# Performance work log

Hardware: AMD Instinct MI355X
Metric: run time of the kernel (lower is better)

The kernel has to match this reference:

```python
import jax, jax.numpy as jnp
import numpy as np

WIN = 4
HEAD_DIM = 32
N_HEADS = 6
TYPE = 'SW'
SHIFT = WIN // 2  # window_size // 2


def _relation():
    # [P, P, 3] relative coordinate indices into the (2w-1)^3 bias table
    cord = np.array([[i, j, k] for i in range(WIN) for j in range(WIN) for k in range(WIN)])
    return cord[:, None, :] - cord[None, :, :] + WIN - 1


def _shift_mask(nw):
    # boolean mask [nw^3, P, P]; True -> -inf (cross-boundary pairs in shifted windows)
    p, s = WIN, WIN - SHIFT
    m = np.zeros((nw, nw, nw, p, p, p, p, p, p), dtype=bool)
    m[-1, :, :, :s, :, :, s:, :, :] = True
    m[-1, :, :, s:, :, :, :s, :, :] = True
    m[:, -1, :, :, :s, :, :, s:, :] = True
    m[:, -1, :, :, s:, :, :, :s, :] = True
    m[:, :, -1, :, :, :s, :, :, s:] = True
    m[:, :, -1, :, :, s:, :, :, :s] = True
    return m.reshape(nw ** 3, p ** 3, p ** 3)


def setup_inputs() -> dict:
    key = jax.random.key(0)
    ks = jax.random.split(key, 6)
    dim = N_HEADS * HEAD_DIM  # 192
    B, S = 2, 32
    x = jax.random.normal(ks[0], (B, S, S, S, dim), jnp.float32)
    W_qkv = jax.random.normal(ks[1], (dim, 3 * dim), jnp.float32) * 0.02
    b_qkv = jnp.zeros((3 * dim,), jnp.float32)
    rel_params = jax.random.normal(ks[2], (N_HEADS, 2 * WIN - 1, 2 * WIN - 1, 2 * WIN - 1), jnp.float32) * 0.02
    W_out = jax.random.normal(ks[3], (dim, dim), jnp.float32) * 0.02
    b_out = jnp.zeros((dim,), jnp.float32)
    return {"x": x, "W_qkv": W_qkv, "b_qkv": b_qkv, "rel_params": rel_params, "W_out": W_out, "b_out": b_out}


def reference(x, W_qkv, b_qkv, rel_params, W_out, b_out):
    B, H, Wd, D, C = x.shape
    p = WIN
    nw = H // p
    scale = HEAD_DIM ** -0.5
    if TYPE != 'W':
        x = jnp.roll(x, (-SHIFT, -SHIFT, -SHIFT), axis=(1, 2, 3))
    # window partition: [B, NW, P, C], NW = nw^3, P = p^3
    xw = x.reshape(B, nw, p, nw, p, nw, p, C).transpose(0, 1, 3, 5, 2, 4, 6, 7).reshape(B, nw ** 3, p ** 3, C)
    qkv = xw @ W_qkv + b_qkv  # [B, NW, P, 3C]
    qkv = qkv.reshape(B, nw ** 3, p ** 3, 3 * N_HEADS, HEAD_DIM).transpose(3, 0, 1, 2, 4)  # [3h, B, NW, P, d]
    q, k, v = qkv[:N_HEADS], qkv[N_HEADS:2 * N_HEADS], qkv[2 * N_HEADS:]
    sim = jnp.einsum('hbwpc,hbwqc->hbwpq', q, k) * scale
    rel = _relation()
    bias = rel_params[:, rel[:, :, 0], rel[:, :, 1], rel[:, :, 2]]  # [h, P, P]
    sim = sim + bias[:, None, None, :, :]
    if TYPE != 'W':
        mask = jnp.asarray(_shift_mask(nw))[None, None]  # [1,1,NW,P,P]
        sim = jnp.where(mask, -jnp.inf, sim)
    probs = jax.nn.softmax(sim, axis=-1)
    out = jnp.einsum('hbwpq,hbwqc->hbwpc', probs, v)
    out = out.transpose(1, 2, 3, 0, 4).reshape(B, nw ** 3, p ** 3, C)  # h b w p c -> b w p (h c)
    out = out @ W_out + b_out
    out = out.reshape(B, nw, nw, nw, p, p, p, C).transpose(0, 1, 4, 2, 5, 3, 6, 7).reshape(B, H, Wd, D, C)
    if TYPE != 'W':
        out = jnp.roll(out, (SHIFT, SHIFT, SHIFT), axis=(1, 2, 3))
    return out
```

## Files before the change

### kernel.cpp

```cpp
#include <hip/hip_runtime.h>

typedef short bf16x8 __attribute__((ext_vector_type(8)));
typedef float f32x4 __attribute__((ext_vector_type(4)));

#define MFMA16(a, b, c) __builtin_amdgcn_mfma_f32_16x16x32_bf16(a, b, c, 0, 0, 0)

__device__ __forceinline__ unsigned short f2bf(float f) {
    unsigned int u = __float_as_uint(f);
    u += 0x7FFFu + ((u >> 16) & 1u);
    return (unsigned short)(u >> 16);
}
__device__ __forceinline__ unsigned int f2bf2(float a, float b) {
    unsigned int ua = __float_as_uint(a);
    ua += 0x7FFFu + ((ua >> 16) & 1u);
    unsigned int ub = __float_as_uint(b);
    ub += 0x7FFFu + ((ub >> 16) & 1u);
    return (ua >> 16) | (ub & 0xFFFF0000u);
}
#define DPPADD(v, CTRL)                                                        \
    {                                                                          \
        int _t = __builtin_amdgcn_mov_dpp(__float_as_int(v), CTRL, 0xf, 0xf, true); \
        v += __int_as_float(_t);                                               \
    }

#define WQT_OFF 0
#define WOT_OFF 221184
#define BQ_OFF  294912

__global__ void prep_kernel(const float* __restrict__ Wqkv,
                            const float* __restrict__ bqkv,
                            const float* __restrict__ Wout,
                            unsigned short* __restrict__ WqT,
                            unsigned short* __restrict__ WoT,
                            float* __restrict__ bq) {
    __shared__ float tile[32][33];
    const float SCALE = 0.17677669529663687f * 1.4426950408889634f;
    int bid = blockIdx.x;
    int tx = threadIdx.x & 31, ty = threadIdx.x >> 5;
    if (bid < 108) {
        int tn = bid % 18, tc = bid / 18;
#pragma unroll
        for (int i = 0; i < 4; ++i)
            tile[ty + i * 8][tx] = Wqkv[(tc * 32 + ty + i * 8) * 576 + tn * 32 + tx];
        __syncthreads();
        bool isQ = (tn < 6);
#pragma unroll
        for (int i = 0; i < 4; ++i) {
            float v = tile[tx][ty + i * 8];
            if (isQ) v *= SCALE;
            WqT[(tn * 32 + ty + i * 8) * 192 + tc * 32 + tx] = f2bf(v);
        }
    } else if (bid < 144) {
        int bb = bid - 108;
        int tn = bb % 6, tc = bb / 6;
#pragma unroll
        for (int i = 0; i < 4; ++i)
            tile[ty + i * 8][tx] = Wout[(tc * 32 + ty + i * 8) * 192 + tn * 32 + tx];
        __syncthreads();
#pragma unroll
        for (int i = 0; i < 4; ++i)
            WoT[(tn * 32 + ty + i * 8) * 192 + tc * 32 + tx] = f2bf(tile[tx][ty + i * 8]);
    } else {
        for (int i = threadIdx.x; i < 576; i += 256) {
            float v = bqkv[i];
            if (i < 192) v *= SCALE;
            bq[i] = v;
        }
    }
}

#define OFF_X   0
#define OFF_P   0
#define OFF_QK  13312
#define OFF_VT  38400
#define OFF_O   52224
#define OFF_RELF 65536
#define SMEM_US 69652

__global__ __launch_bounds__(512) void wmsa_kernel(
    const float* __restrict__ x, const float* __restrict__ rel,
    const float* __restrict__ bout,
    const unsigned short* __restrict__ WqT,
    const unsigned short* __restrict__ WoT,
    const float* __restrict__ bq, float* __restrict__ out) {
    __shared__ __align__(16) unsigned short smem[SMEM_US];
    float* sRel = (float*)&smem[OFF_RELF];

    const int tid = threadIdx.x;
    const int bw = blockIdx.x;
    const int b  = bw >> 9;
    const int w  = bw & 511;
    const int wz = w >> 6, wy = (w >> 3) & 7, wx = w & 7;

    const int lane = tid & 63;
    const int wv   = tid >> 6;
    const int g    = lane >> 4;
    const int l15  = lane & 15;

    for (int i = tid; i < 2058; i += 512) sRel[i] = rel[i] * 1.4426950408889634f;
    {
        int t = tid >> 3, q8 = tid & 7;
        int tz = t >> 4, ty = (t >> 2) & 3, tx = t & 3;
        int gz = (wz * 4 + tz + 2) & 31;
        int gy = (wy * 4 + ty + 2) & 31;
        int gx = (wx * 4 + tx + 2) & 31;
        const float* xp = x + ((((b * 32 + gz) * 32 + gy) * 32 + gx)) * 192;
#pragma unroll
        for (int k = 0; k < 6; ++k) {
            int c = (q8 << 2) + (k << 5);
            float4 v = *(const float4*)(xp + c);
            uint2 pk;
            pk.x = f2bf2(v.x, v.y);
            pk.y = f2bf2(v.z, v.w);
            *(uint2*)&smem[OFF_X + t * 208 + c] = pk;
        }
    }

    int nb = wv;
    float bias = bq[nb * 16 + l15];
    bf16x8 bfr[6];
    {
        const unsigned short* wp = WqT + (nb * 16 + l15) * 192 + g * 8;
#pragma unroll
        for (int kk = 0; kk < 6; ++kk) bfr[kk] = *(const bf16x8*)(wp + kk * 32);
    }
    __syncthreads();

    {
        bf16x8 afr[4][6];
#pragma unroll
        for (int m = 0; m < 4; ++m)
#pragma unroll
            for (int kk = 0; kk < 6; ++kk)
                afr[m][kk] = *(const bf16x8*)&smem[OFF_X + (m * 16 + l15) * 208 + kk * 32 + g * 8];

        while (true) {
            int nbN = nb + 8;
            bool more = (nbN < 36);
            bf16x8 bfrN[6];
            float biasN = 0.f;
            if (more) {
                biasN = bq[nbN * 16 + l15];
                const unsigned short* wp = WqT + (nbN * 16 + l15) * 192 + g * 8;
#pragma unroll
                for (int kk = 0; kk < 6; ++kk) bfrN[kk] = *(const bf16x8*)(wp + kk * 32);
            }
            int colg = nb * 16 + l15;
            bool isV = (nb >= 24);
#pragma unroll
            for (int m = 0; m < 4; ++m) {
                f32x4 acc = {bias, bias, bias, bias};
#pragma unroll
                for (int kk = 0; kk < 6; ++kk) acc = MFMA16(afr[m][kk], bfr[kk], acc);
                int row0 = m * 16 + g * 4;
                unsigned int u01 = f2bf2(acc[0], acc[1]);
                unsigned int u23 = f2bf2(acc[2], acc[3]);
                if (!isV) {
                    unsigned short* qk = &smem[OFF_QK + row0 * 392 + colg];
                    qk[0]    = (unsigned short)u01;
                    qk[392]  = (unsigned short)(u01 >> 16);
                    qk[784]  = (unsigned short)u23;
                    qk[1176] = (unsigned short)(u23 >> 16);
                } else {
                    uint2 pk; pk.x = u01; pk.y = u23;
                    *(uint2*)&smem[OFF_VT + (colg - 384) * 72 + row0] = pk;
                }
            }
            if (!more) break;
            nb = nbN;
            bias = biasN;
#pragma unroll
            for (int kk = 0; kk < 6; ++kk) bfr[kk] = bfrN[kk];
        }
    }
    __syncthreads();

    const bool sz = (wz == 7), sy = (wy == 7), sx = (wx == 7);
    {
        const int qy = (l15 >> 2) & 3, qx = l15 & 3;
        unsigned short* pb = &smem[OFF_P + wv * 1152];
        for (int it = wv * 3; it < wv * 3 + 3; ++it) {
            int h = it >> 2, mb = it & 3;
            bf16x8 qf = *(const bf16x8*)&smem[OFF_QK + (mb * 16 + l15) * 392 + h * 32 + g * 8];
            f32x4 s[4];
#pragma unroll
            for (int f = 0; f < 4; ++f) {
                bf16x8 kf = *(const bf16x8*)&smem[OFF_QK + (f * 16 + l15) * 392 + 192 + h * 32 + g * 8];
                f32x4 z = {0.f, 0.f, 0.f, 0.f};
                s[f] = MFMA16(qf, kf, z);
            }
#pragma unroll
            for (int f = 0; f < 4; ++f) {
                bool mz = sz && ((mb < 2) != (f < 2));
                bool my = sy && ((g < 2) != (qy < 2));
                int base = h * 343 + (mb - f + 3) * 49 + (g - qy + 3) * 7 + (3 - qx);
#pragma unroll
                for (int r = 0; r < 4; ++r) {
                    float v = s[f][r] + sRel[base + r];
                    bool mx = sx && ((r < 2) != (qx < 2));
                    v = (mz | my | mx) ? -1e30f : v;
                    s[f][r] = exp2f(v);
                }
            }
            float inv[4];
#pragma unroll
            for (int r = 0; r < 4; ++r) {
                float sm = (s[0][r] + s[1][r]) + (s[2][r] + s[3][r]);
                DPPADD(sm, 0xB1);
                DPPADD(sm, 0x4E);
                DPPADD(sm, 0x124);
                DPPADD(sm, 0x128);
                inv[r] = __builtin_amdgcn_rcpf(sm);
            }
#pragma unroll
            for (int f = 0; f < 4; ++f) {
                unsigned int u01 = f2bf2(s[f][0], s[f][1]);
                unsigned int u23 = f2bf2(s[f][2], s[f][3]);
                unsigned short* pw = &pb[(g * 4) * 72 + f * 16 + l15];
                pw[0]   = (unsigned short)u01;
                pw[72]  = (unsigned short)(u01 >> 16);
                pw[144] = (unsigned short)u23;
                pw[216] = (unsigned short)(u23 >> 16);
            }
            f32x4 o0 = {0.f, 0.f, 0.f, 0.f}, o1 = {0.f, 0.f, 0.f, 0.f};
#pragma unroll
            for (int kt = 0; kt < 2; ++kt) {
                bf16x8 pf = *(const bf16x8*)&pb[l15 * 72 + kt * 32 + g * 8];
                bf16x8 v0 = *(const bf16x8*)&smem[OFF_VT + (h * 32 + l15) * 72 + kt * 32 + g * 8];
                bf16x8 v1 = *(const bf16x8*)&smem[OFF_VT + (h * 32 + 16 + l15) * 72 + kt * 32 + g * 8];
                o0 = MFMA16(pf, v0, o0);
                o1 = MFMA16(pf, v1, o1);
            }
#pragma unroll
            for (int r = 0; r < 4; ++r) { o0[r] *= inv[r]; o1[r] *= inv[r]; }
            unsigned int a0 = f2bf2(o0[0], o0[1]), a1 = f2bf2(o0[2], o0[3]);
            unsigned int c0 = f2bf2(o1[0], o1[1]), c1 = f2bf2(o1[2], o1[3]);
            unsigned short* ow = &smem[OFF_O + (mb * 16 + g * 4) * 208 + h * 32 + l15];
            ow[0]        = (unsigned short)a0;
            ow[208]      = (unsigned short)(a0 >> 16);
            ow[416]      = (unsigned short)a1;
            ow[624]      = (unsigned short)(a1 >> 16);
            ow[16]       = (unsigned short)c0;
            ow[16 + 208] = (unsigned short)(c0 >> 16);
            ow[16 + 416] = (unsigned short)c1;
            ow[16 + 624] = (unsigned short)(c1 >> 16);
        }
    }

    const int mw = wv >> 2, nq = wv & 3;
    int col0 = nq * 16 + l15;
    float bo0 = bout[col0];
    bf16x8 bfr0[6];
    {
        const unsigned short* wp = WoT + col0 * 192 + g * 8;
#pragma unroll
        for (int kk = 0; kk < 6; ++kk) bfr0[kk] = *(const bf16x8*)(wp + kk * 32);
    }
    __syncthreads();

    {
        bf16x8 ofr[2][6];
#pragma unroll
        for (int mi = 0; mi < 2; ++mi)
#pragma unroll
            for (int kk = 0; kk < 6; ++kk)
                ofr[mi][kk] = *(const bf16x8*)&smem[OFF_O + ((mw * 2 + mi) * 16 + l15) * 208 + kk * 32 + g * 8];
#pragma unroll
        for (int nbi = 0; nbi < 3; ++nbi) {
            int col = (nq + nbi * 4) * 16 + l15;
            float bo;
            bf16x8 bfr[6];
            if (nbi == 0) {
                bo = bo0;
#pragma unroll
                for (int kk = 0; kk < 6; ++kk) bfr[kk] = bfr0[kk];
            } else {
                bo = bout[col];
                const unsigned short* wp = WoT + col * 192 + g * 8;
#pragma unroll
                for (int kk = 0; kk < 6; ++kk) bfr[kk] = *(const bf16x8*)(wp + kk * 32);
            }
#pragma unroll
            for (int mi = 0; mi < 2; ++mi) {
                f32x4 acc = {bo, bo, bo, bo};
#pragma unroll
                for (int kk = 0; kk < 6; ++kk) acc = MFMA16(ofr[mi][kk], bfr[kk], acc);
                int m = mw * 2 + mi;
                int gz = (wz * 4 + m + 2) & 31;
                int gy = (wy * 4 + g + 2) & 31;
#pragma unroll
                for (int r = 0; r < 4; ++r) {
                    int gx = (wx * 4 + r + 2) & 31;
                    out[(((b * 32 + gz) * 32 + gy) * 32 + gx) * 192 + col] = acc[r];
                }
            }
        }
    }
}

extern "C" void kernel_launch(void* const* d_in, const int* in_sizes, int n_in,
                              void* d_out, int out_size, void* d_ws, size_t ws_size,
                              hipStream_t stream) {
    const float* x    = (const float*)d_in[0];
    const float* Wqkv = (const float*)d_in[1];
    const float* bqkv = (const float*)d_in[2];
    const float* rel  = (const float*)d_in[3];
    const float* Wout = (const float*)d_in[4];
    const float* bout = (const float*)d_in[5];

    unsigned short* WqT = (unsigned short*)((char*)d_ws + WQT_OFF);
    unsigned short* WoT = (unsigned short*)((char*)d_ws + WOT_OFF);
    float*          bq  = (float*)((char*)d_ws + BQ_OFF);
    float*          out = (float*)d_out;

    prep_kernel<<<145, 256, 0, stream>>>(Wqkv, bqkv, Wout, WqT, WoT, bq);
    wmsa_kernel<<<1024, 512, 0, stream>>>(x, rel, bout, WqT, WoT, bq, out);
}
```

Baseline: 166.7 us.

## Precompute per-lane bias table, swap MFMA operands, shrink LDS for two blocks per CU

Adds a prep stage that expands the relative-position bias into a per-lane table in global memory, so each block no longer loads the rel table into LDS and the inner loop reads contiguous float4s. The QKV and output GEMMs swap MFMA operand order so accumulators map to contiguous columns, which gives vectorized LDS stores and float4 global output stores instead of scattered scalar stores. Softmax normalization moves before the PV product. X is stored in a fragment-friendly layout, and LDS use drops to allow two 512-thread blocks per CU via launch bounds. The cost is extra global bias-table traffic, per-block reads of that table, and tighter register limits.

```diff
diff --git a/kernel.cpp b/kernel.cpp
--- a/kernel.cpp
+++ b/kernel.cpp
@@ -26,14 +26,18 @@
 #define WQT_OFF 0
 #define WOT_OFF 221184
 #define BQ_OFF  294912
+#define TBL_OFF 297216
 
 __global__ void prep_kernel(const float* __restrict__ Wqkv,
                             const float* __restrict__ bqkv,
                             const float* __restrict__ Wout,
+                            const float* __restrict__ rel,
                             unsigned short* __restrict__ WqT,
                             unsigned short* __restrict__ WoT,
-                            float* __restrict__ bq) {
+                            float* __restrict__ bq,
+                            float* __restrict__ tblB) {
     __shared__ float tile[32][33];
+    const float LOG2E = 1.4426950408889634f;
     const float SCALE = 0.17677669529663687f * 1.4426950408889634f;
     int bid = blockIdx.x;
     int tx = threadIdx.x & 31, ty = threadIdx.x >> 5;
@@ -60,31 +64,36 @@
 #pragma unroll
         for (int i = 0; i < 4; ++i)
             WoT[(tn * 32 + ty + i * 8) * 192 + tc * 32 + tx] = f2bf(tile[tx][ty + i * 8]);
-    } else {
+    } else if (bid == 144) {
         for (int i = threadIdx.x; i < 576; i += 256) {
             float v = bqkv[i];
             if (i < 192) v *= SCALE;
             bq[i] = v;
         }
+    } else {
+        int e = (bid - 145) * 256 + threadIdx.x;
+        int r = e & 3, f = (e >> 2) & 3;
+        int lane = (e >> 4) & 63, mb = (e >> 10) & 3, h = e >> 12;
+        int g = lane >> 4, l15 = lane & 15;
+        int qy = l15 >> 2, qx = l15 & 3;
+        int dz = mb - f + 3, dy = g - qy + 3, dx = r - qx + 3;
+        tblB[e] = rel[((h * 7 + dz) * 7 + dy) * 7 + dx] * LOG2E;
     }
 }
 
 #define OFF_X   0
-#define OFF_P   0
-#define OFF_QK  13312
-#define OFF_VT  38400
-#define OFF_O   52224
-#define OFF_RELF 65536
-#define SMEM_US 69652
-
-__global__ __launch_bounds__(512) void wmsa_kernel(
-    const float* __restrict__ x, const float* __restrict__ rel,
+#define OFF_QK  12288
+#define OFF_VT  37376
+#define OFF_O   51200
+#define SMEM_US 64000
+
+__global__ __launch_bounds__(512, 2) void wmsa_kernel(
+    const float* __restrict__ x, const float* __restrict__ tblB,
     const float* __restrict__ bout,
     const unsigned short* __restrict__ WqT,
     const unsigned short* __restrict__ WoT,
     const float* __restrict__ bq, float* __restrict__ out) {
     __shared__ __align__(16) unsigned short smem[SMEM_US];
-    float* sRel = (float*)&smem[OFF_RELF];
 
     const int tid = threadIdx.x;
     const int bw = blockIdx.x;
@@ -97,7 +106,6 @@
     const int g    = lane >> 4;
     const int l15  = lane & 15;
 
-    for (int i = tid; i < 2058; i += 512) sRel[i] = rel[i] * 1.4426950408889634f;
     {
         int t = tid >> 3, q8 = tid & 7;
         int tz = t >> 4, ty = (t >> 2) & 3, tx = t & 3;
@@ -105,80 +113,86 @@
         int gy = (wy * 4 + ty + 2) & 31;
         int gx = (wx * 4 + tx + 2) & 31;
         const float* xp = x + ((((b * 32 + gz) * 32 + gy) * 32 + gx)) * 192;
+        int g0 = q8 >> 1, j0 = (q8 & 1) * 4, lt = t & 15;
 #pragma unroll
         for (int k = 0; k < 6; ++k) {
-            int c = (q8 << 2) + (k << 5);
-            float4 v = *(const float4*)(xp + c);
+            float4 v = *(const float4*)(xp + q8 * 4 + k * 32);
             uint2 pk;
             pk.x = f2bf2(v.x, v.y);
             pk.y = f2bf2(v.z, v.w);
-            *(uint2*)&smem[OFF_X + t * 208 + c] = pk;
+            *(uint2*)&smem[OFF_X + ((((k * 4 + g0) * 4 + tz) * 16 + lt) * 8) + j0] = pk;
         }
     }
 
     int nb = wv;
-    float bias = bq[nb * 16 + l15];
-    bf16x8 bfr[6];
+    bf16x8 wfr[6];
     {
         const unsigned short* wp = WqT + (nb * 16 + l15) * 192 + g * 8;
 #pragma unroll
-        for (int kk = 0; kk < 6; ++kk) bfr[kk] = *(const bf16x8*)(wp + kk * 32);
+        for (int kk = 0; kk < 6; ++kk) wfr[kk] = *(const bf16x8*)(wp + kk * 32);
     }
     __syncthreads();
 
     {
-        bf16x8 afr[4][6];
-#pragma unroll
-        for (int m = 0; m < 4; ++m)
+        bf16x8 xfr[4][6];
+#pragma unroll
+        for (int tb = 0; tb < 4; ++tb)
 #pragma unroll
             for (int kk = 0; kk < 6; ++kk)
-                afr[m][kk] = *(const bf16x8*)&smem[OFF_X + (m * 16 + l15) * 208 + kk * 32 + g * 8];
+                xfr[tb][kk] = *(const bf16x8*)&smem[OFF_X + (((kk * 4 + g) * 4 + tb) * 16 + l15) * 8];
 
         while (true) {
             int nbN = nb + 8;
             bool more = (nbN < 36);
-            bf16x8 bfrN[6];
-            float biasN = 0.f;
+            bf16x8 wfrN[6];
             if (more) {
-                biasN = bq[nbN * 16 + l15];
                 const unsigned short* wp = WqT + (nbN * 16 + l15) * 192 + g * 8;
 #pragma unroll
-                for (int kk = 0; kk < 6; ++kk) bfrN[kk] = *(const bf16x8*)(wp + kk * 32);
-            }
-            int colg = nb * 16 + l15;
-            bool isV = (nb >= 24);
-#pragma unroll
-            for (int m = 0; m < 4; ++m) {
-                f32x4 acc = {bias, bias, bias, bias};
-#pragma unroll
-                for (int kk = 0; kk < 6; ++kk) acc = MFMA16(afr[m][kk], bfr[kk], acc);
-                int row0 = m * 16 + g * 4;
-                unsigned int u01 = f2bf2(acc[0], acc[1]);
-                unsigned int u23 = f2bf2(acc[2], acc[3]);
-                if (!isV) {
-                    unsigned short* qk = &smem[OFF_QK + row0 * 392 + colg];
-                    qk[0]    = (unsigned short)u01;
-                    qk[392]  = (unsigned short)(u01 >> 16);
-                    qk[784]  = (unsigned short)u23;
-                    qk[1176] = (unsigned short)(u23 >> 16);
-                } else {
-                    uint2 pk; pk.x = u01; pk.y = u23;
-                    *(uint2*)&smem[OFF_VT + (colg - 384) * 72 + row0] = pk;
+                for (int kk = 0; kk < 6; ++kk) wfrN[kk] = *(const bf16x8*)(wp + kk * 32);
+            }
+            if (nb < 24) {
+                f32x4 bqv = *(const f32x4*)(bq + nb * 16 + g * 4);
+                int qkcol = (nb < 12) ? nb * 16 : 192 + (nb - 12) * 16;
+#pragma unroll
+                for (int tb = 0; tb < 4; ++tb) {
+                    f32x4 acc = bqv;
+#pragma unroll
+                    for (int kk = 0; kk < 6; ++kk) acc = MFMA16(wfr[kk], xfr[tb][kk], acc);
+                    uint2 pk;
+                    pk.x = f2bf2(acc[0], acc[1]);
+                    pk.y = f2bf2(acc[2], acc[3]);
+                    *(uint2*)&smem[OFF_QK + (tb * 16 + l15) * 392 + qkcol + g * 4] = pk;
+                }
+            } else {
+                float bs = bq[nb * 16 + l15];
+                int c = (nb - 24) * 16 + l15;
+#pragma unroll
+                for (int tb = 0; tb < 4; ++tb) {
+                    f32x4 acc = {bs, bs, bs, bs};
+#pragma unroll
+                    for (int kk = 0; kk < 6; ++kk) acc = MFMA16(xfr[tb][kk], wfr[kk], acc);
+                    uint2 pk;
+                    pk.x = f2bf2(acc[0], acc[1]);
+                    pk.y = f2bf2(acc[2], acc[3]);
+                    *(uint2*)&smem[OFF_VT + c * 72 + tb * 16 + g * 4] = pk;
                 }
             }
             if (!more) break;
             nb = nbN;
-            bias = biasN;
-#pragma unroll
-            for (int kk = 0; kk < 6; ++kk) bfr[kk] = bfrN[kk];
+#pragma unroll
+            for (int kk = 0; kk < 6; ++kk) wfr[kk] = wfrN[kk];
         }
     }
     __syncthreads();
 
     const bool sz = (wz == 7), sy = (wy == 7), sx = (wx == 7);
     {
-        const int qy = (l15 >> 2) & 3, qx = l15 & 3;
-        unsigned short* pb = &smem[OFF_P + wv * 1152];
+        const int qy = l15 >> 2, qx = l15 & 3;
+        const bool my = sy && ((g < 2) != (qy < 2));
+        bool mxr[4];
+#pragma unroll
+        for (int r = 0; r < 4; ++r) mxr[r] = sx && ((r < 2) != (qx < 2));
+        unsigned short* pb = &smem[OFF_X + wv * 1152];
         for (int it = wv * 3; it < wv * 3 + 3; ++it) {
             int h = it >> 2, mb = it & 3;
             bf16x8 qf = *(const bf16x8*)&smem[OFF_QK + (mb * 16 + l15) * 392 + h * 32 + g * 8];
@@ -189,16 +203,15 @@
                 f32x4 z = {0.f, 0.f, 0.f, 0.f};
                 s[f] = MFMA16(qf, kf, z);
             }
+            const f32x4* tp = (const f32x4*)(tblB + ((h * 4 + mb) * 64 + lane) * 16);
 #pragma unroll
             for (int f = 0; f < 4; ++f) {
-                bool mz = sz && ((mb < 2) != (f < 2));
-                bool my = sy && ((g < 2) != (qy < 2));
-                int base = h * 343 + (mb - f + 3) * 49 + (g - qy + 3) * 7 + (3 - qx);
+                f32x4 bv = tp[f];
+                bool mzy = (sz && ((mb < 2) != (f < 2))) | my;
 #pragma unroll
                 for (int r = 0; r < 4; ++r) {
-                    float v = s[f][r] + sRel[base + r];
-                    bool mx = sx && ((r < 2) != (qx < 2));
-                    v = (mz | my | mx) ? -1e30f : v;
+                    float v = s[f][r] + bv[r];
+                    v = (mzy | mxr[r]) ? -1e30f : v;
                     s[f][r] = exp2f(v);
                 }
             }
@@ -214,8 +227,8 @@
             }
 #pragma unroll
             for (int f = 0; f < 4; ++f) {
-                unsigned int u01 = f2bf2(s[f][0], s[f][1]);
-                unsigned int u23 = f2bf2(s[f][2], s[f][3]);
+                unsigned int u01 = f2bf2(s[f][0] * inv[0], s[f][1] * inv[1]);
+                unsigned int u23 = f2bf2(s[f][2] * inv[2], s[f][3] * inv[3]);
                 unsigned short* pw = &pb[(g * 4) * 72 + f * 16 + l15];
                 pw[0]   = (unsigned short)u01;
                 pw[72]  = (unsigned short)(u01 >> 16);
@@ -228,72 +241,52 @@
                 bf16x8 pf = *(const bf16x8*)&pb[l15 * 72 + kt * 32 + g * 8];
                 bf16x8 v0 = *(const bf16x8*)&smem[OFF_VT + (h * 32 + l15) * 72 + kt * 32 + g * 8];
                 bf16x8 v1 = *(const bf16x8*)&smem[OFF_VT + (h * 32 + 16 + l15) * 72 + kt * 32 + g * 8];
-                o0 = MFMA16(pf, v0, o0);
-                o1 = MFMA16(pf, v1, o1);
-            }
-#pragma unroll
-            for (int r = 0; r < 4; ++r) { o0[r] *= inv[r]; o1[r] *= inv[r]; }
-            unsigned int a0 = f2bf2(o0[0], o0[1]), a1 = f2bf2(o0[2], o0[3]);
-            unsigned int c0 = f2bf2(o1[0], o1[1]), c1 = f2bf2(o1[2], o1[3]);
-            unsigned short* ow = &smem[OFF_O + (mb * 16 + g * 4) * 208 + h * 32 + l15];
-            ow[0]        = (unsigned short)a0;
-            ow[208]      = (unsigned short)(a0 >> 16);
-            ow[416]      = (unsigned short)a1;
-            ow[624]      = (unsigned short)(a1 >> 16);
-            ow[16]       = (unsigned short)c0;
-            ow[16 + 208] = (unsigned short)(c0 >> 16);
-            ow[16 + 416] = (unsigned short)c1;
-            ow[16 + 624] = (unsigned short)(c1 >> 16);
-        }
-    }
-
-    const int mw = wv >> 2, nq = wv & 3;
-    int col0 = nq * 16 + l15;
-    float bo0 = bout[col0];
-    bf16x8 bfr0[6];
-    {
-        const unsigned short* wp = WoT + col0 * 192 + g * 8;
-#pragma unroll
-        for (int kk = 0; kk < 6; ++kk) bfr0[kk] = *(const bf16x8*)(wp + kk * 32);
+                o0 = MFMA16(v0, pf, o0);
+                o1 = MFMA16(v1, pf, o1);
+            }
+            uint2 p0, p1;
+            p0.x = f2bf2(o0[0], o0[1]); p0.y = f2bf2(o0[2], o0[3]);
+            p1.x = f2bf2(o1[0], o1[1]); p1.y = f2bf2(o1[2], o1[3]);
+            int oi = OFF_O + (mb * 16 + l15) * 200 + h * 32 + g * 4;
+            *(uint2*)&smem[oi]      = p0;
+            *(uint2*)&smem[oi + 16] = p1;
+        }
+    }
+
+    const int tb3 = wv >> 1, nb0 = (wv & 1) * 6;
+    bf16x8 w3[6];
+    {
+        const unsigned short* wp = WoT + (nb0 * 16 + l15) * 192 + g * 8;
+#pragma unroll
+        for (int kk = 0; kk < 6; ++kk) w3[kk] = *(const bf16x8*)(wp + kk * 32);
     }
     __syncthreads();
 
     {
-        bf16x8 ofr[2][6];
-#pragma unroll
-        for (int mi = 0; mi < 2; ++mi)
-#pragma unroll
-            for (int kk = 0; kk < 6; ++kk)
-                ofr[mi][kk] = *(const bf16x8*)&smem[OFF_O + ((mw * 2 + mi) * 16 + l15) * 208 + kk * 32 + g * 8];
-#pragma unroll
-        for (int nbi = 0; nbi < 3; ++nbi) {
-            int col = (nq + nbi * 4) * 16 + l15;
-            float bo;
-            bf16x8 bfr[6];
-            if (nbi == 0) {
-                bo = bo0;
-#pragma unroll
-                for (int kk = 0; kk < 6; ++kk) bfr[kk] = bfr0[kk];
+        bf16x8 ofr[6];
+#pragma unroll
+        for (int kk = 0; kk < 6; ++kk)
+            ofr[kk] = *(const bf16x8*)&smem[OFF_O + (tb3 * 16 + l15) * 200 + kk * 32 + g * 8];
+        const int gz = (wz * 4 + tb3 + 2) & 31;
+        const int gy = (wy * 4 + (l15 >> 2) + 2) & 31;
+        const int gx = (wx * 4 + (l15 & 3) + 2) & 31;
+        float* op = out + ((((b * 32 + gz) * 32 + gy) * 32 + gx)) * 192;
+#pragma unroll
+        for (int u = 0; u < 6; ++u) {
+            int nb3 = nb0 + u;
+            bf16x8 wf[6];
+            if (u == 0) {
+#pragma unroll
+                for (int kk = 0; kk < 6; ++kk) wf[kk] = w3[kk];
             } else {
-                bo = bout[col];
-                const unsigned short* wp = WoT + col * 192 + g * 8;
-#pragma unroll
-                for (int kk = 0; kk < 6; ++kk) bfr[kk] = *(const bf16x8*)(wp + kk * 32);
-            }
-#pragma unroll
-            for (int mi = 0; mi < 2; ++mi) {
-                f32x4 acc = {bo, bo, bo, bo};
-#pragma unroll
-                for (int kk = 0; kk < 6; ++kk) acc = MFMA16(ofr[mi][kk], bfr[kk], acc);
-                int m = mw * 2 + mi;
-                int gz = (wz * 4 + m + 2) & 31;
-                int gy = (wy * 4 + g + 2) & 31;
-#pragma unroll
-                for (int r = 0; r < 4; ++r) {
-                    int gx = (wx * 4 + r + 2) & 31;
-                    out[(((b * 32 + gz) * 32 + gy) * 32 + gx) * 192 + col] = acc[r];
-                }
-            }
+                const unsigned short* wp = WoT + (nb3 * 16 + l15) * 192 + g * 8;
+#pragma unroll
+                for (int kk = 0; kk < 6; ++kk) wf[kk] = *(const bf16x8*)(wp + kk * 32);
+            }
+            f32x4 acc = *(const f32x4*)(bout + nb3 * 16 + g * 4);
+#pragma unroll
+            for (int kk = 0; kk < 6; ++kk) acc = MFMA16(wf[kk], ofr[kk], acc);
+            *(f32x4*)(op + nb3 * 16 + g * 4) = acc;
         }
     }
 }
@@ -311,8 +304,9 @@
     unsigned short* WqT = (unsigned short*)((char*)d_ws + WQT_OFF);
     unsigned short* WoT = (unsigned short*)((char*)d_ws + WOT_OFF);
     float*          bq  = (float*)((char*)d_ws + BQ_OFF);
+    float*          tbl = (float*)((char*)d_ws + TBL_OFF);
     float*          out = (float*)d_out;
 
-    prep_kernel<<<145, 256, 0, stream>>>(Wqkv, bqkv, Wout, WqT, WoT, bq);
-    wmsa_kernel<<<1024, 512, 0, stream>>>(x, rel, bout, WqT, WoT, bq, out);
-}
+    prep_kernel<<<241, 256, 0, stream>>>(Wqkv, bqkv, Wout, rel, WqT, WoT, bq, tbl);
+    wmsa_kernel<<<1024, 512, 0, stream>>>(x, tbl, bout, WqT, WoT, bq, out);
+}
```

Result: slower. 188.8 us (+13.3%).

## Precompute lane-ordered relative bias table and swizzle X tile layout in LDS

Applied to the files above, without the earlier changes.

The prep kernel now expands the relative-position bias into a per-lane, per-fragment table (scaled by log2e) in workspace. The attention stage reads it with vector global loads instead of gathering from an LDS copy built per block. The X tile in LDS is reordered into a fragment-contiguous layout so A-fragment reads avoid padded strided access, and the LDS footprint shrinks. Mask predicates are hoisted and the output-projection weight loads are software-pipelined one block ahead. In exchange there are extra global reads of a 24K-float table, and the prep kernel does more work.

```diff
diff --git a/kernel.cpp b/kernel.cpp
--- a/kernel.cpp
+++ b/kernel.cpp
@@ -26,14 +26,18 @@
 #define WQT_OFF 0
 #define WOT_OFF 221184
 #define BQ_OFF  294912
+#define TBL_OFF 297216
 
 __global__ void prep_kernel(const float* __restrict__ Wqkv,
                             const float* __restrict__ bqkv,
                             const float* __restrict__ Wout,
+                            const float* __restrict__ rel,
                             unsigned short* __restrict__ WqT,
                             unsigned short* __restrict__ WoT,
-                            float* __restrict__ bq) {
+                            float* __restrict__ bq,
+                            float* __restrict__ tblB) {
     __shared__ float tile[32][33];
+    const float LOG2E = 1.4426950408889634f;
     const float SCALE = 0.17677669529663687f * 1.4426950408889634f;
     int bid = blockIdx.x;
     int tx = threadIdx.x & 31, ty = threadIdx.x >> 5;
@@ -60,31 +64,37 @@
 #pragma unroll
         for (int i = 0; i < 4; ++i)
             WoT[(tn * 32 + ty + i * 8) * 192 + tc * 32 + tx] = f2bf(tile[tx][ty + i * 8]);
-    } else {
+    } else if (bid == 144) {
         for (int i = threadIdx.x; i < 576; i += 256) {
             float v = bqkv[i];
             if (i < 192) v *= SCALE;
             bq[i] = v;
         }
+    } else {
+        int e = (bid - 145) * 256 + threadIdx.x;
+        int r = e & 3, f = (e >> 2) & 3;
+        int lane = (e >> 4) & 63, mb = (e >> 10) & 3, h = e >> 12;
+        int g = lane >> 4, l15 = lane & 15;
+        int qy = l15 >> 2, qx = l15 & 3;
+        int dz = mb - f + 3, dy = g - qy + 3, dx = r - qx + 3;
+        tblB[e] = rel[((h * 7 + dz) * 7 + dy) * 7 + dx] * LOG2E;
     }
 }
 
 #define OFF_X   0
 #define OFF_P   0
-#define OFF_QK  13312
-#define OFF_VT  38400
-#define OFF_O   52224
-#define OFF_RELF 65536
-#define SMEM_US 69652
+#define OFF_QK  12288
+#define OFF_VT  37376
+#define OFF_O   51200
+#define SMEM_US 64512
 
 __global__ __launch_bounds__(512) void wmsa_kernel(
-    const float* __restrict__ x, const float* __restrict__ rel,
+    const float* __restrict__ x, const float* __restrict__ tblB,
     const float* __restrict__ bout,
     const unsigned short* __restrict__ WqT,
     const unsigned short* __restrict__ WoT,
     const float* __restrict__ bq, float* __restrict__ out) {
     __shared__ __align__(16) unsigned short smem[SMEM_US];
-    float* sRel = (float*)&smem[OFF_RELF];
 
     const int tid = threadIdx.x;
     const int bw = blockIdx.x;
@@ -97,7 +107,6 @@
     const int g    = lane >> 4;
     const int l15  = lane & 15;
 
-    for (int i = tid; i < 2058; i += 512) sRel[i] = rel[i] * 1.4426950408889634f;
     {
         int t = tid >> 3, q8 = tid & 7;
         int tz = t >> 4, ty = (t >> 2) & 3, tx = t & 3;
@@ -105,14 +114,14 @@
         int gy = (wy * 4 + ty + 2) & 31;
         int gx = (wx * 4 + tx + 2) & 31;
         const float* xp = x + ((((b * 32 + gz) * 32 + gy) * 32 + gx)) * 192;
+        int g0 = q8 >> 1, j0 = (q8 & 1) * 4, lt = t & 15;
 #pragma unroll
         for (int k = 0; k < 6; ++k) {
-            int c = (q8 << 2) + (k << 5);
-            float4 v = *(const float4*)(xp + c);
+            float4 v = *(const float4*)(xp + q8 * 4 + k * 32);
             uint2 pk;
             pk.x = f2bf2(v.x, v.y);
             pk.y = f2bf2(v.z, v.w);
-            *(uint2*)&smem[OFF_X + t * 208 + c] = pk;
+            *(uint2*)&smem[OFF_X + ((((k * 4 + g0) * 4 + tz) * 16 + lt) * 8) + j0] = pk;
         }
     }
 
@@ -132,7 +141,7 @@
         for (int m = 0; m < 4; ++m)
 #pragma unroll
             for (int kk = 0; kk < 6; ++kk)
-                afr[m][kk] = *(const bf16x8*)&smem[OFF_X + (m * 16 + l15) * 208 + kk * 32 + g * 8];
+                afr[m][kk] = *(const bf16x8*)&smem[OFF_X + (((kk * 4 + g) * 4 + m) * 16 + l15) * 8];
 
         while (true) {
             int nbN = nb + 8;
@@ -177,10 +186,18 @@
 
     const bool sz = (wz == 7), sy = (wy == 7), sx = (wx == 7);
     {
-        const int qy = (l15 >> 2) & 3, qx = l15 & 3;
+        const int qy = l15 >> 2, qx = l15 & 3;
+        const bool my = sy && ((g < 2) != (qy < 2));
+        bool mxr[4];
+#pragma unroll
+        for (int r = 0; r < 4; ++r) mxr[r] = sx && ((r < 2) != (qx < 2));
         unsigned short* pb = &smem[OFF_P + wv * 1152];
         for (int it = wv * 3; it < wv * 3 + 3; ++it) {
             int h = it >> 2, mb = it & 3;
+            const f32x4* tp = (const f32x4*)(tblB + ((h * 4 + mb) * 64 + lane) * 16);
+            f32x4 bv[4];
+#pragma unroll
+            for (int f = 0; f < 4; ++f) bv[f] = tp[f];
             bf16x8 qf = *(const bf16x8*)&smem[OFF_QK + (mb * 16 + l15) * 392 + h * 32 + g * 8];
             f32x4 s[4];
 #pragma unroll
@@ -191,14 +208,11 @@
             }
 #pragma unroll
             for (int f = 0; f < 4; ++f) {
-                bool mz = sz && ((mb < 2) != (f < 2));
-                bool my = sy && ((g < 2) != (qy < 2));
-                int base = h * 343 + (mb - f + 3) * 49 + (g - qy + 3) * 7 + (3 - qx);
+                bool mzy = (sz && ((mb < 2) != (f < 2))) | my;
 #pragma unroll
                 for (int r = 0; r < 4; ++r) {
-                    float v = s[f][r] + sRel[base + r];
-                    bool mx = sx && ((r < 2) != (qx < 2));
-                    v = (mz | my | mx) ? -1e30f : v;
+                    float v = s[f][r] + bv[f][r];
+                    v = (mzy | mxr[r]) ? -1e30f : v;
                     s[f][r] = exp2f(v);
                 }
             }
@@ -249,12 +263,12 @@
 
     const int mw = wv >> 2, nq = wv & 3;
     int col0 = nq * 16 + l15;
-    float bo0 = bout[col0];
-    bf16x8 bfr0[6];
+    float boc = bout[col0];
+    bf16x8 bfr3[6];
     {
         const unsigned short* wp = WoT + col0 * 192 + g * 8;
 #pragma unroll
-        for (int kk = 0; kk < 6; ++kk) bfr0[kk] = *(const bf16x8*)(wp + kk * 32);
+        for (int kk = 0; kk < 6; ++kk) bfr3[kk] = *(const bf16x8*)(wp + kk * 32);
     }
     __syncthreads();
 
@@ -268,23 +282,20 @@
 #pragma unroll
         for (int nbi = 0; nbi < 3; ++nbi) {
             int col = (nq + nbi * 4) * 16 + l15;
-            float bo;
-            bf16x8 bfr[6];
-            if (nbi == 0) {
-                bo = bo0;
-#pragma unroll
-                for (int kk = 0; kk < 6; ++kk) bfr[kk] = bfr0[kk];
-            } else {
-                bo = bout[col];
-                const unsigned short* wp = WoT + col * 192 + g * 8;
-#pragma unroll
-                for (int kk = 0; kk < 6; ++kk) bfr[kk] = *(const bf16x8*)(wp + kk * 32);
+            float boN = 0.f;
+            bf16x8 bfrN[6];
+            if (nbi < 2) {
+                int colN = (nq + (nbi + 1) * 4) * 16 + l15;
+                boN = bout[colN];
+                const unsigned short* wp = WoT + colN * 192 + g * 8;
+#pragma unroll
+                for (int kk = 0; kk < 6; ++kk) bfrN[kk] = *(const bf16x8*)(wp + kk * 32);
             }
 #pragma unroll
             for (int mi = 0; mi < 2; ++mi) {
-                f32x4 acc = {bo, bo, bo, bo};
-#pragma unroll
-                for (int kk = 0; kk < 6; ++kk) acc = MFMA16(ofr[mi][kk], bfr[kk], acc);
+                f32x4 acc = {boc, boc, boc, boc};
+#pragma unroll
+                for (int kk = 0; kk < 6; ++kk) acc = MFMA16(ofr[mi][kk], bfr3[kk], acc);
                 int m = mw * 2 + mi;
                 int gz = (wz * 4 + m + 2) & 31;
                 int gy = (wy * 4 + g + 2) & 31;
@@ -294,6 +305,9 @@
                     out[(((b * 32 + gz) * 32 + gy) * 32 + gx) * 192 + col] = acc[r];
                 }
             }
+            boc = boN;
+#pragma unroll
+            for (int kk = 0; kk < 6; ++kk) bfr3[kk] = bfrN[kk];
         }
     }
 }
@@ -311,8 +325,9 @@
     unsigned short* WqT = (unsigned short*)((char*)d_ws + WQT_OFF);
     unsigned short* WoT = (unsigned short*)((char*)d_ws + WOT_OFF);
     float*          bq  = (float*)((char*)d_ws + BQ_OFF);
+    float*          tbl = (float*)((char*)d_ws + TBL_OFF);
     float*          out = (float*)d_out;
 
-    prep_kernel<<<145, 256, 0, stream>>>(Wqkv, bqkv, Wout, WqT, WoT, bq);
-    wmsa_kernel<<<1024, 512, 0, stream>>>(x, rel, bout, WqT, WoT, bq, out);
-}
+    prep_kernel<<<241, 256, 0, stream>>>(Wqkv, bqkv, Wout, rel, WqT, WoT, bq, tbl);
+    wmsa_kernel<<<1024, 512, 0, stream>>>(x, tbl, bout, WqT, WoT, bq, out);
+}
```

Result: no change. 163.7 us (-1.8%).
